# Optimization experiments

Measured on AMD Instinct MI355X. Metric: run time of the kernel, lower is better.

## Reference

```python
import jax, jax.numpy as jnp
import numpy as np

B, STATE_DIM, MLP_DIM, H, W = 128, 64, 512, 40, 40
LN_EPS = 1e-5


def _sobel_kernel(c):
    # Per-channel depthwise filters in torch order: [c0_sx, c0_sy, c0_id, c1_sx, ...]
    sx = jnp.array([[-1., 0., 1.], [-2., 0., 2.], [-1., 0., 1.]], jnp.float32)
    sy = jnp.array([[-1., -2., -1.], [0., 0., 0.], [1., 2., 1.]], jnp.float32)
    ident = jnp.array([[0., 0., 0.], [0., 1., 0.], [0., 0., 0.]], jnp.float32)
    k = jnp.stack([sx, sy, ident])[:, None]      # [3, 1, 3, 3]
    return jnp.tile(k, (c, 1, 1, 1))             # [3c, 1, 3, 3]


def setup_inputs() -> dict:
    key = jax.random.key(0)
    ks = jax.random.split(key, 6)
    state_in = jax.random.normal(ks[0], (B, STATE_DIM, H, W), jnp.float32)
    w1 = jax.random.normal(ks[1], (MLP_DIM, 3 * STATE_DIM), jnp.float32) * 0.05
    ln_weight = jax.random.uniform(ks[2], (MLP_DIM, H, W), jnp.float32, 0.5, 1.5)
    ln_bias = jax.random.normal(ks[3], (MLP_DIM, H, W), jnp.float32) * 0.01
    w2 = jax.random.normal(ks[4], (STATE_DIM, MLP_DIM), jnp.float32) * 0.05
    mask = jax.random.randint(ks[5], (H, W), 0, 2, jnp.int32)  # bernoulli(0.5) update mask
    return {"state_in": state_in, "w1": w1, "ln_weight": ln_weight,
            "ln_bias": ln_bias, "w2": w2, "mask": mask}


def reference(state_in, w1, ln_weight, ln_bias, w2, mask):
    C = state_in.shape[1]
    # Depthwise 3x3 sobel/identity perception: [B, C, H, W] -> [B, 3C, H, W]
    kern = _sobel_kernel(C)
    x = jax.lax.conv_general_dilated(
        state_in, kern, window_strides=(1, 1), padding='SAME',
        dimension_numbers=('NCHW', 'OIHW', 'NCHW'), feature_group_count=C)
    # 1x1 conv (no bias): [B, 3C, H, W] -> [B, MLP, H, W]
    x = jnp.einsum('bchw,oc->bohw', x, w1)
    # LayerNorm over (MLP, H, W) per sample, with elementwise affine
    mu = jnp.mean(x, axis=(1, 2, 3), keepdims=True)
    var = jnp.var(x, axis=(1, 2, 3), keepdims=True)
    x = (x - mu) * jax.lax.rsqrt(var + LN_EPS) * ln_weight + ln_bias
    x = jax.nn.relu(x)
    # 1x1 conv back to state channels (zero-init in original; random here for testing)
    x = jnp.einsum('bchw,oc->bohw', x, w2)
    # Stochastic per-pixel update mask, broadcast over batch and channels
    x = x * mask.astype(jnp.float32)
    # Alive mask: 3x3 max-pool on alive channel, stride 1, SAME padding
    live = jax.lax.reduce_window(state_in[:, 3], -jnp.inf, jax.lax.max,
                                 (1, 3, 3), (1, 1, 1), 'SAME')
    live = (live > 0.1).astype(jnp.float32)[:, None]  # [B, 1, H, W]
    return state_in + x * live
```

## Files before the change

### kernel.cpp

```cpp
#include <hip/hip_runtime.h>


typedef unsigned short u16;
typedef unsigned int   u32;
typedef __attribute__((ext_vector_type(8))) u16    ushort8;
typedef __attribute__((ext_vector_type(4))) u16    u16x4;
typedef __attribute__((ext_vector_type(8))) __bf16 bf16x8;
typedef __attribute__((ext_vector_type(4))) float  f32x4;
typedef __attribute__((ext_vector_type(4))) u32    u32x4;

#define NB   128
#define NC   64
#define K1   192
#define NO   512
#define NHW  1600
#define LN_N 819200.0f

__device__ __forceinline__ u16 f2bf(float f) {
    union { float f; u32 u; } v; v.f = f;
    u32 u = v.u;
    u32 r = u + 0x7fffu + ((u >> 16) & 1u);
    return (u16)(r >> 16);
}
__device__ __forceinline__ float bf2f(u16 h) {
    union { u32 u; float f; } v; v.u = ((u32)h) << 16; return v.f;
}
__device__ __forceinline__ float bfhi(u32 c) {
    union { u32 u; float f; } v; v.u = c & 0xffff0000u; return v.f;
}
__device__ __forceinline__ float bflo(u32 c) {
    union { u32 u; float f; } v; v.u = c << 16; return v.f;
}
__device__ __forceinline__ f32x4 mfma16(bf16x8 a, bf16x8 b, f32x4 c) {
    return __builtin_amdgcn_mfma_f32_16x16x32_bf16(a, b, c, 0, 0, 0);
}
__device__ __forceinline__ bf16x8 ldfrag(const u16* p) {
    return *(const bf16x8*)p;
}

__device__ __forceinline__ void load_halo(const float* __restrict__ base, int h,
                                          int wq, float reg[3][12]) {
#pragma unroll
    for (int jj = 0; jj < 3; ++jj) {
        int hh = h + jj - 1;
        bool vh = (unsigned)hh < 40u;
        const float* rowp = base + hh * 40;
#pragma unroll
        for (int i = 0; i < 12; ++i) {
            int col = wq * 10 - 1 + i;
            reg[jj][i] = (vh && (unsigned)col < 40u) ? rowp[col] : 0.0f;
        }
    }
}
__device__ __forceinline__ void sobel_px(const float reg[3][12], int t,
                                         float& sx, float& sy, float& idn) {
    sx = (reg[0][t + 2] - reg[0][t]) + 2.0f * (reg[1][t + 2] - reg[1][t])
       + (reg[2][t + 2] - reg[2][t]);
    sy = (reg[2][t] + 2.0f * reg[2][t + 1] + reg[2][t + 2])
       - (reg[0][t] + 2.0f * reg[0][t + 1] + reg[0][t + 2]);
    idn = reg[1][t + 1];
}

__global__ __launch_bounds__(256) void k0_convert(const float* __restrict__ w1,
                                                  const float* __restrict__ w2,
                                                  u16* __restrict__ w1p,
                                                  u16* __restrict__ w1T,
                                                  u16* __restrict__ w2p,
                                                  float* __restrict__ stats) {
    int g = blockIdx.x * 256 + threadIdx.x;
    if (g < NO * K1) {
        u16 v = f2bf(w1[g]);
        int o = g / K1, k = g - o * K1;
        int f = o >> 4, ks = k >> 5;
        int lane = (((k >> 3) & 3) << 4) | (o & 15);
        w1p[(size_t)(((f * 6 + ks) * 64 + lane) * 8 + (k & 7))] = v;
        w1T[(size_t)k * NO + o] = v;
    } else if (g < NO * K1 + NC * NO) {
        int i = g - NO * K1;
        int s = i / NO, o = i - s * NO;
        u16 v = f2bf(w2[i]);
        int wid = s >> 4, oc = o >> 6, ks2 = (o >> 5) & 1;
        int lane = (((o >> 3) & 3) << 4) | (s & 15);
        w2p[(size_t)((((wid * 8 + oc) * 2 + ks2) * 64 + lane) * 8 + (o & 7))] = v;
    } else if (g < NO * K1 + NC * NO + 256) {
        stats[g - NO * K1 - NC * NO] = 0.0f;
    }
}

__global__ __launch_bounds__(256) void k0_lncomb(const float* __restrict__ lnw,
                                                 const float* __restrict__ lnb,
                                                 u32* __restrict__ lnp) {
    int g = blockIdx.x * 256 + threadIdx.x;
    int r = g & 3;
    int lane = (g >> 2) & 63;
    int rest = g >> 8;
    int mi = rest % 5;  rest /= 5;
    int wid = rest & 3; rest >>= 2;
    int oc = rest & 7;
    int bx = rest >> 3;
    int p = bx * 80 + mi * 16 + (lane & 15);
    int o = oc * 64 + wid * 16 + ((lane >> 4) << 2) + r;
    size_t gi = (size_t)o * NHW + p;
    lnp[g] = ((u32)f2bf(lnb[gi]) << 16) | f2bf(lnw[gi]);
}

__global__ __launch_bounds__(256) void k0_gram(const u16* __restrict__ w1T,
                                               float* __restrict__ G,
                                               float* __restrict__ colw1) {
    const int blk = blockIdx.x;
    const int tid = threadIdx.x;
    const int lane = tid & 63, wid = tid >> 6;
    const int q = lane >> 4, l15 = lane & 15;
    if (blk < 36) {
        int bj = blk / 6, bk = blk - bj * 6;
        int j0 = bj * 32 + (wid & 1) * 16, k0 = bk * 32 + (wid >> 1) * 16;
        f32x4 acc = {0.f, 0.f, 0.f, 0.f};
#pragma unroll
        for (int ks = 0; ks < 16; ++ks) {
            bf16x8 a  = ldfrag(&w1T[(size_t)(j0 + l15) * NO + ks * 32 + q * 8]);
            bf16x8 bb = ldfrag(&w1T[(size_t)(k0 + l15) * NO + ks * 32 + q * 8]);
            acc = mfma16(a, bb, acc);
        }
#pragma unroll
        for (int r = 0; r < 4; ++r)
            G[(size_t)(j0 + q * 4 + r) * K1 + k0 + l15] = acc[r];
    } else if (tid < K1) {
        float s = 0.f;
        for (int i = 0; i < NO / 8; ++i) {
            ushort8 v = *(const ushort8*)&w1T[(size_t)tid * NO + i * 8];
#pragma unroll
            for (int j = 0; j < 8; ++j) s += bf2f(v[j]);
        }
        colw1[tid] = s;
    }
}

__global__ __launch_bounds__(256) void k2_stats(const float* __restrict__ state,
                                                const float* __restrict__ G,
                                                const float* __restrict__ colw1,
                                                float* __restrict__ stats) {
    const int b = blockIdx.x >> 2, quarter = blockIdx.x & 3;
    const int tid = threadIdx.x;
    const int lane = tid & 63, wid = tid >> 6;
    const int q = lane >> 4, l15 = lane & 15;
    const int j0 = (wid & 1) * 96, j1 = (wid >> 1) * 96, jo = wid * 48;

    __shared__ __align__(16) u16 Pt[208 * 104];
    __shared__ float red[8];

    for (int i = tid; i < 208 * 104 / 2; i += 256) ((u32*)Pt)[i] = 0u;
    __syncthreads();
    if (tid < 80) Pt[192 * 104 + tid] = 0x3F80u;

    f32x4 acc[6][6], accO[3];
#pragma unroll
    for (int i = 0; i < 6; ++i)
#pragma unroll
        for (int j = 0; j < 6; ++j) { f32x4 z = {0.f,0.f,0.f,0.f}; acc[i][j] = z; }
#pragma unroll
    for (int j = 0; j < 3; ++j) { f32x4 z = {0.f,0.f,0.f,0.f}; accO[j] = z; }

    const int c = tid >> 2, wq = tid & 3;
    const float* base = state + ((size_t)b * NC + c) * NHW;

    for (int tile = 0; tile < 5; ++tile) {
        const int h0 = (quarter * 5 + tile) * 2;
        __syncthreads();
        for (int rr = 0; rr < 2; ++rr) {
            float reg[3][12];
            load_halo(base, h0 + rr, wq, reg);
#pragma unroll
            for (int t = 0; t < 10; ++t) {
                float sx, sy, idn; sobel_px(reg, t, sx, sy, idn);
                int px = rr * 40 + wq * 10 + t;
                Pt[(3 * c + 0) * 104 + px] = f2bf(sx);
                Pt[(3 * c + 1) * 104 + px] = f2bf(sy);
                Pt[(3 * c + 2) * 104 + px] = f2bf(idn);
            }
        }
        __syncthreads();
#pragma unroll
        for (int ks = 0; ks < 3; ++ks) {
            bf16x8 av[6], bv[6], ao, bo[3];
#pragma unroll
            for (int fi = 0; fi < 6; ++fi)
                av[fi] = ldfrag(&Pt[(j0 + fi * 16 + l15) * 104 + ks * 32 + q * 8]);
#pragma unroll
            for (int fj = 0; fj < 6; ++fj)
                bv[fj] = ldfrag(&Pt[(j1 + fj * 16 + l15) * 104 + ks * 32 + q * 8]);
            ao = ldfrag(&Pt[(192 + l15) * 104 + ks * 32 + q * 8]);
#pragma unroll
            for (int fj = 0; fj < 3; ++fj)
                bo[fj] = ldfrag(&Pt[(jo + fj * 16 + l15) * 104 + ks * 32 + q * 8]);
#pragma unroll
            for (int fi = 0; fi < 6; ++fi)
#pragma unroll
                for (int fj = 0; fj < 6; ++fj)
                    acc[fi][fj] = mfma16(av[fi], bv[fj], acc[fi][fj]);
#pragma unroll
            for (int fj = 0; fj < 3; ++fj)
                accO[fj] = mfma16(ao, bo[fj], accO[fj]);
        }
    }

    float ssq = 0.f;
#pragma unroll
    for (int fi = 0; fi < 6; ++fi)
#pragma unroll
        for (int fj = 0; fj < 6; ++fj) {
            f32x4 gv = *(const f32x4*)&G[(size_t)(j1 + fj * 16 + l15) * K1
                                         + j0 + fi * 16 + q * 4];
#pragma unroll
            for (int r = 0; r < 4; ++r) ssq += acc[fi][fj][r] * gv[r];
        }
    float sm = 0.f;
    if (q == 0) {
#pragma unroll
        for (int fj = 0; fj < 3; ++fj)
            sm += accO[fj][0] * colw1[jo + fj * 16 + l15];
    }
#pragma unroll
    for (int off = 32; off > 0; off >>= 1) {
        ssq += __shfl_down(ssq, off);
        sm  += __shfl_down(sm, off);
    }
    if (lane == 0) { red[wid] = ssq; red[4 + wid] = sm; }
    __syncthreads();
    if (tid == 0) {
        atomicAdd(&stats[b * 2],     red[4] + red[5] + red[6] + red[7]);
        atomicAdd(&stats[b * 2 + 1], red[0] + red[1] + red[2] + red[3]);
    }
}

__global__ void k3_finalize(const float* __restrict__ stats, float2* __restrict__ musig) {
    int t = threadIdx.x;
    if (t < NB) {
        float s = stats[2 * t], qq = stats[2 * t + 1];
        float inv = 1.0f / LN_N;
        float mu = s * inv;
        float var = qq * inv - mu * mu;
        float2 r; r.x = mu; r.y = rsqrtf(var + 1e-5f);
        musig[t] = r;
    }
}

__global__ __launch_bounds__(256, 4) void k4_fused(const float* __restrict__ state,
                                                   const u16* __restrict__ w1p,
                                                   const u16* __restrict__ w2p,
                                                   const u32* __restrict__ lnp,
                                                   const int* __restrict__ mask,
                                                   const float2* __restrict__ musig,
                                                   float* __restrict__ out) {
    const int bx = blockIdx.x;
    const int b  = blockIdx.y;
    const int p0 = bx * 80, h0 = bx * 2;
    const int tid = threadIdx.x;
    const int lane = tid & 63, wid = tid >> 6;
    const int q = lane >> 4, l15 = lane & 15;

    __shared__ __align__(16) u16 Pt[80 * 192];
    __shared__ __align__(16) u16 Ys[80 * 64];

    const float2 ms = musig[b];
    const float mu = ms.x, rs = ms.y;
    const float murs = mu * rs;

    {
        const int c = tid >> 2, wq = tid & 3;
        const float* base = state + ((size_t)b * NC + c) * NHW;
        for (int rr = 0; rr < 2; ++rr) {
            float reg[3][12];
            load_halo(base, h0 + rr, wq, reg);
#pragma unroll
            for (int t = 0; t < 10; ++t) {
                float sx, sy, idn; sobel_px(reg, t, sx, sy, idn);
                int px = rr * 40 + wq * 10 + t;
                int k = 3 * c;
#pragma unroll
                for (int i = 0; i < 3; ++i) {
                    int kk = k + i, u = kk >> 3;
                    int elem = px * 192 + (((u & 0x18) | ((u ^ px) & 7)) << 3) + (kk & 7);
                    Pt[elem] = f2bf(i == 0 ? sx : (i == 1 ? sy : idn));
                }
            }
        }
    }
    float g5[5];
    {
        const float* st3 = state + ((size_t)b * NC + 3) * NHW;
#pragma unroll
        for (int mi = 0; mi < 5; ++mi) {
            int p = p0 + mi * 16 + l15;
            int h = p / 40, w = p - h * 40;
            float mx = -1e30f;
#pragma unroll
            for (int dh = -1; dh <= 1; ++dh) {
                int hh = h + dh;
                if ((unsigned)hh < 40u)
#pragma unroll
                    for (int dw = -1; dw <= 1; ++dw) {
                        int wc = w + dw;
                        if ((unsigned)wc < 40u) mx = fmaxf(mx, st3[hh * 40 + wc]);
                    }
            }
            g5[mi] = (mx > 0.1f && mask[p] != 0) ? 1.0f : 0.0f;
        }
    }
    __syncthreads();

    f32x4 acc2[5];
#pragma unroll
    for (int i = 0; i < 5; ++i) { f32x4 z = {0.f,0.f,0.f,0.f}; acc2[i] = z; }

    for (int oc = 0; oc < 8; ++oc) {
        u32x4 lv[5];
        {
            const u32* lb = lnp + ((((size_t)bx * 8 + oc) * 4 + wid) * 5) * 256 + lane * 4;
#pragma unroll
            for (int mi = 0; mi < 5; ++mi)
                lv[mi] = *(const u32x4*)(lb + mi * 256);
        }
        const u16* w2base = w2p + ((size_t)(wid * 8 + oc) * 2) * 512 + lane * 8;
        bf16x8 aw0 = ldfrag(w2base);
        bf16x8 aw1 = ldfrag(w2base + 512);

        f32x4 acc1[5];
#pragma unroll
        for (int i = 0; i < 5; ++i) { f32x4 z = {0.f,0.f,0.f,0.f}; acc1[i] = z; }
        const u16* w1base = w1p + ((size_t)(oc * 4 + wid) * 6) * 512 + lane * 8;
#pragma unroll
        for (int ks = 0; ks < 6; ++ks) {
            bf16x8 a = ldfrag(w1base + ks * 512);
#pragma unroll
            for (int mi = 0; mi < 5; ++mi) {
                int r = mi * 16 + l15, u = ks * 4 + q;
                bf16x8 bp = ldfrag(&Pt[r * 192 + (((u & 0x18) | ((u ^ r) & 7)) << 3)]);
                acc1[mi] = mfma16(a, bp, acc1[mi]);
            }
        }
#pragma unroll
        for (int mi = 0; mi < 5; ++mi) {
            int p = mi * 16 + l15;
            u16x4 yv;
#pragma unroll
            for (int r = 0; r < 4; ++r) {
                u32 cc = lv[mi][r];
                float t = fmaf(acc1[mi][r], rs, -murs);
                float y = fmaf(t, bflo(cc), bfhi(cc));
                yv[r] = f2bf(fmaxf(y, 0.0f));
            }
            int u = wid * 2 + (q >> 1);
            int up = u ^ (p & 7);
            *(u16x4*)&Ys[p * 64 + up * 8 + (q & 1) * 4] = yv;
        }
        __syncthreads();
#pragma unroll
        for (int ks2 = 0; ks2 < 2; ++ks2) {
            bf16x8 aw = ks2 ? aw1 : aw0;
#pragma unroll
            for (int mi = 0; mi < 5; ++mi) {
                int p = mi * 16 + l15;
                int u = ks2 * 4 + q;
                int up = u ^ (p & 7);
                bf16x8 by = ldfrag(&Ys[p * 64 + up * 8]);
                acc2[mi] = mfma16(aw, by, acc2[mi]);
            }
        }
        __syncthreads();
    }

#pragma unroll
    for (int mi = 0; mi < 5; ++mi) {
        int p = p0 + mi * 16 + l15;
        float g = g5[mi];
#pragma unroll
        for (int r = 0; r < 4; ++r) {
            int s = wid * 16 + q * 4 + r;
            size_t idx = ((size_t)b * NC + s) * NHW + p;
            out[idx] = state[idx] + g * acc2[mi][r];
        }
    }
}

extern "C" void kernel_launch(void* const* d_in, const int* in_sizes, int n_in,
                              void* d_out, int out_size, void* d_ws, size_t ws_size,
                              hipStream_t stream) {
    const float* state = (const float*)d_in[0];
    const float* w1    = (const float*)d_in[1];
    const float* lnw   = (const float*)d_in[2];
    const float* lnb   = (const float*)d_in[3];
    const float* w2    = (const float*)d_in[4];
    const int*   mask  = (const int*)d_in[5];
    float* out = (float*)d_out;

    char* ws = (char*)d_ws;
    u16*    w1p   = (u16*)(ws + 0ull);
    u16*    w2p   = (u16*)(ws + 196608ull);
    u32*    lnp   = (u32*)(ws + 262144ull);
    u16*    w1T   = (u16*)(ws + 3538944ull);
    float*  G     = (float*)(ws + 3735552ull);
    float*  colw1 = (float*)(ws + 3883008ull);
    float*  stats = (float*)(ws + 3883776ull);
    float2* musig = (float2*)(ws + 3884800ull);

    k0_convert <<<513, 256, 0, stream>>>(w1, w2, w1p, w1T, w2p, stats);
    k0_lncomb  <<<3200, 256, 0, stream>>>(lnw, lnb, lnp);
    k0_gram    <<<37, 256, 0, stream>>>(w1T, G, colw1);
    k2_stats   <<<512, 256, 0, stream>>>(state, G, colw1, stats);
    k3_finalize<<<1, 128, 0, stream>>>(stats, musig);
    k4_fused   <<<dim3(20, 128), 256, 0, stream>>>(state, w1p, w2p, lnp,
                                                   mask, musig, out);
}
```

Measured before the change: 300.8 us.

## Split second GEMM K across waves with per-wave Y tiles and LDS reduction

Each wave now keeps its own 16-channel slice of the hidden activations in a private LDS tile and computes partial products for all 64 output channels. This removes the two block-wide barriers per output-chunk iteration, and the partial sums are reduced through LDS at the end. The w2 layout and a zero-fill kernel are changed to match. The alive-mask computation moves to the epilogue. The cost is four times as many accumulator registers (80 floats), which risks occupancy loss under the 4-block launch bound, plus an extra cross-wave reduction.

```diff
diff --git a/kernel.cpp b/kernel.cpp
--- a/kernel.cpp
+++ b/kernel.cpp
@@ -61,11 +61,16 @@
     idn = reg[1][t + 1];
 }
 
+__global__ __launch_bounds__(256) void k0_zero(u32* __restrict__ w2q32) {
+    int i = blockIdx.x * 256 + threadIdx.x;
+    if (i < 32768) w2q32[i] = 0u;
+}
+
 __global__ __launch_bounds__(256) void k0_convert(const float* __restrict__ w1,
                                                   const float* __restrict__ w2,
                                                   u16* __restrict__ w1p,
                                                   u16* __restrict__ w1T,
-                                                  u16* __restrict__ w2p,
+                                                  u16* __restrict__ w2q,
                                                   float* __restrict__ stats) {
     int g = blockIdx.x * 256 + threadIdx.x;
     if (g < NO * K1) {
@@ -77,11 +82,13 @@
         w1T[(size_t)k * NO + o] = v;
     } else if (g < NO * K1 + NC * NO) {
         int i = g - NO * K1;
-        int s = i / NO, o = i - s * NO;
+        int s = i >> 9, o = i & 511;
         u16 v = f2bf(w2[i]);
-        int wid = s >> 4, oc = o >> 6, ks2 = (o >> 5) & 1;
-        int lane = (((o >> 3) & 3) << 4) | (s & 15);
-        w2p[(size_t)((((wid * 8 + oc) * 2 + ks2) * 64 + lane) * 8 + (o & 7))] = v;
+        int oc = o >> 6, wid = (o >> 4) & 3, k = o & 15;
+        int qq = k >> 3, j = o & 7;
+        int lane = qq * 16 + (s & 15);
+        int sf = s >> 4;
+        w2q[((((size_t)(oc * 4 + sf) * 4 + wid) * 64 + lane) << 3) + j] = v;
     } else if (g < NO * K1 + NC * NO + 256) {
         stats[g - NO * K1 - NC * NO] = 0.0f;
     }
@@ -246,7 +253,7 @@
 
 __global__ __launch_bounds__(256, 4) void k4_fused(const float* __restrict__ state,
                                                    const u16* __restrict__ w1p,
-                                                   const u16* __restrict__ w2p,
+                                                   const u16* __restrict__ w2q,
                                                    const u32* __restrict__ lnp,
                                                    const int* __restrict__ mask,
                                                    const float2* __restrict__ musig,
@@ -258,8 +265,10 @@
     const int lane = tid & 63, wid = tid >> 6;
     const int q = lane >> 4, l15 = lane & 15;
 
-    __shared__ __align__(16) u16 Pt[80 * 192];
-    __shared__ __align__(16) u16 Ys[80 * 64];
+    __shared__ __align__(16) char smem[40960];
+    u16* Pt  = (u16*)smem;
+    u16* Ysw = (u16*)(smem + 30720) + wid * 1280;
+    float* Rd = (float*)smem;
 
     const float2 ms = musig[b];
     const float mu = ms.x, rs = ms.y;
@@ -285,99 +294,180 @@
             }
         }
     }
-    float g5[5];
-    {
-        const float* st3 = state + ((size_t)b * NC + 3) * NHW;
-#pragma unroll
-        for (int mi = 0; mi < 5; ++mi) {
-            int p = p0 + mi * 16 + l15;
-            int h = p / 40, w = p - h * 40;
-            float mx = -1e30f;
-#pragma unroll
-            for (int dh = -1; dh <= 1; ++dh) {
-                int hh = h + dh;
-                if ((unsigned)hh < 40u)
-#pragma unroll
-                    for (int dw = -1; dw <= 1; ++dw) {
-                        int wc = w + dw;
-                        if ((unsigned)wc < 40u) mx = fmaxf(mx, st3[hh * 40 + wc]);
-                    }
-            }
-            g5[mi] = (mx > 0.1f && mask[p] != 0) ? 1.0f : 0.0f;
-        }
-    }
-    __syncthreads();
-
-    f32x4 acc2[5];
-#pragma unroll
-    for (int i = 0; i < 5; ++i) { f32x4 z = {0.f,0.f,0.f,0.f}; acc2[i] = z; }
+    __syncthreads();
+
+    f32x4 acc2[4][5];
+#pragma unroll
+    for (int sf = 0; sf < 4; ++sf)
+#pragma unroll
+        for (int i = 0; i < 5; ++i) { f32x4 z = {0.f,0.f,0.f,0.f}; acc2[sf][i] = z; }
+
+    const int swz = (((l15 >> 2) ^ l15) & 1);
 
     for (int oc = 0; oc < 8; ++oc) {
-        u32x4 lv[5];
+        const u16* w1base = w1p + ((size_t)(oc * 4 + wid) * 6) * 512 + lane * 8;
+        const u32* lbase = lnp + ((((size_t)bx * 8 + oc) * 4 + wid) * 5) * 256 + lane * 4;
+
         {
-            const u32* lb = lnp + ((((size_t)bx * 8 + oc) * 4 + wid) * 5) * 256 + lane * 4;
-#pragma unroll
-            for (int mi = 0; mi < 5; ++mi)
-                lv[mi] = *(const u32x4*)(lb + mi * 256);
-        }
-        const u16* w2base = w2p + ((size_t)(wid * 8 + oc) * 2) * 512 + lane * 8;
-        bf16x8 aw0 = ldfrag(w2base);
-        bf16x8 aw1 = ldfrag(w2base + 512);
-
-        f32x4 acc1[5];
-#pragma unroll
-        for (int i = 0; i < 5; ++i) { f32x4 z = {0.f,0.f,0.f,0.f}; acc1[i] = z; }
-        const u16* w1base = w1p + ((size_t)(oc * 4 + wid) * 6) * 512 + lane * 8;
-#pragma unroll
-        for (int ks = 0; ks < 6; ++ks) {
-            bf16x8 a = ldfrag(w1base + ks * 512);
-#pragma unroll
-            for (int mi = 0; mi < 5; ++mi) {
-                int r = mi * 16 + l15, u = ks * 4 + q;
-                bf16x8 bp = ldfrag(&Pt[r * 192 + (((u & 0x18) | ((u ^ r) & 7)) << 3)]);
-                acc1[mi] = mfma16(a, bp, acc1[mi]);
-            }
-        }
-#pragma unroll
-        for (int mi = 0; mi < 5; ++mi) {
-            int p = mi * 16 + l15;
-            u16x4 yv;
-#pragma unroll
-            for (int r = 0; r < 4; ++r) {
-                u32 cc = lv[mi][r];
-                float t = fmaf(acc1[mi][r], rs, -murs);
-                float y = fmaf(t, bflo(cc), bfhi(cc));
-                yv[r] = f2bf(fmaxf(y, 0.0f));
-            }
-            int u = wid * 2 + (q >> 1);
-            int up = u ^ (p & 7);
-            *(u16x4*)&Ys[p * 64 + up * 8 + (q & 1) * 4] = yv;
-        }
-        __syncthreads();
-#pragma unroll
-        for (int ks2 = 0; ks2 < 2; ++ks2) {
-            bf16x8 aw = ks2 ? aw1 : aw0;
+            f32x4 acc1[3];
+#pragma unroll
+            for (int i = 0; i < 3; ++i) { f32x4 z = {0.f,0.f,0.f,0.f}; acc1[i] = z; }
+#pragma unroll
+            for (int ks = 0; ks < 6; ++ks) {
+                bf16x8 a = ldfrag(w1base + (ks << 9));
+#pragma unroll
+                for (int mi = 0; mi < 3; ++mi) {
+                    int r = mi * 16 + l15, u = ks * 4 + q;
+                    bf16x8 bp = ldfrag(&Pt[r * 192 + (((u & 0x18) | ((u ^ r) & 7)) << 3)]);
+                    acc1[mi] = mfma16(a, bp, acc1[mi]);
+                }
+            }
+#pragma unroll
+            for (int mi = 0; mi < 3; ++mi) {
+                u32x4 lv = *(const u32x4*)(lbase + mi * 256);
+                u16x4 yv;
+#pragma unroll
+                for (int r = 0; r < 4; ++r) {
+                    u32 cc = lv[r];
+                    float t = fmaf(acc1[mi][r], rs, -murs);
+                    float y = fmaf(t, bflo(cc), bfhi(cc));
+                    yv[r] = f2bf(fmaxf(y, 0.0f));
+                }
+                int p = mi * 16 + l15;
+                *(u16x4*)&Ysw[p * 16 + (((q >> 1) ^ swz) << 3) + ((q & 1) << 2)] = yv;
+            }
+        }
+        {
+            f32x4 acc1[2];
+#pragma unroll
+            for (int i = 0; i < 2; ++i) { f32x4 z = {0.f,0.f,0.f,0.f}; acc1[i] = z; }
+#pragma unroll
+            for (int ks = 0; ks < 6; ++ks) {
+                bf16x8 a = ldfrag(w1base + (ks << 9));
+#pragma unroll
+                for (int mi = 0; mi < 2; ++mi) {
+                    int r = (mi + 3) * 16 + l15, u = ks * 4 + q;
+                    bf16x8 bp = ldfrag(&Pt[r * 192 + (((u & 0x18) | ((u ^ r) & 7)) << 3)]);
+                    acc1[mi] = mfma16(a, bp, acc1[mi]);
+                }
+            }
+#pragma unroll
+            for (int mi = 0; mi < 2; ++mi) {
+                u32x4 lv = *(const u32x4*)(lbase + (mi + 3) * 256);
+                u16x4 yv;
+#pragma unroll
+                for (int r = 0; r < 4; ++r) {
+                    u32 cc = lv[r];
+                    float t = fmaf(acc1[mi][r], rs, -murs);
+                    float y = fmaf(t, bflo(cc), bfhi(cc));
+                    yv[r] = f2bf(fmaxf(y, 0.0f));
+                }
+                int p = (mi + 3) * 16 + l15;
+                *(u16x4*)&Ysw[p * 16 + (((q >> 1) ^ swz) << 3) + ((q & 1) << 2)] = yv;
+            }
+        }
+        {
+            bf16x8 aw0 = ldfrag(w2q + (((size_t)(oc * 4 + 0) * 4 + wid) << 9) + lane * 8);
+            bf16x8 aw1 = ldfrag(w2q + (((size_t)(oc * 4 + 1) * 4 + wid) << 9) + lane * 8);
+            bf16x8 aw2 = ldfrag(w2q + (((size_t)(oc * 4 + 2) * 4 + wid) << 9) + lane * 8);
+            bf16x8 aw3 = ldfrag(w2q + (((size_t)(oc * 4 + 3) * 4 + wid) << 9) + lane * 8);
 #pragma unroll
             for (int mi = 0; mi < 5; ++mi) {
                 int p = mi * 16 + l15;
-                int u = ks2 * 4 + q;
-                int up = u ^ (p & 7);
-                bf16x8 by = ldfrag(&Ys[p * 64 + up * 8]);
-                acc2[mi] = mfma16(aw, by, acc2[mi]);
-            }
-        }
-        __syncthreads();
-    }
-
+                bf16x8 by = ldfrag(&Ysw[p * 16 + ((((q & 1) ^ swz)) << 3)]);
+                acc2[0][mi] = mfma16(aw0, by, acc2[0][mi]);
+                acc2[1][mi] = mfma16(aw1, by, acc2[1][mi]);
+                acc2[2][mi] = mfma16(aw2, by, acc2[2][mi]);
+                acc2[3][mi] = mfma16(aw3, by, acc2[3][mi]);
+            }
+        }
+    }
+
+    __syncthreads();
+#pragma unroll
+    for (int sf = 0; sf < 2; ++sf) {
+        if (wid != sf) {
+#pragma unroll
+            for (int mi = 0; mi < 5; ++mi)
+                *(f32x4*)(Rd + (size_t)(sf * 4 + wid) * 1280 + mi * 256 + lane * 4)
+                    = acc2[sf][mi];
+        }
+    }
+    __syncthreads();
+#pragma unroll
+    for (int sf = 0; sf < 2; ++sf) {
+        if (wid == sf) {
+#pragma unroll
+            for (int w = 0; w < 4; ++w) {
+                if (w == sf) continue;
+#pragma unroll
+                for (int mi = 0; mi < 5; ++mi) {
+                    f32x4 v = *(const f32x4*)(Rd + (size_t)(sf * 4 + w) * 1280
+                                              + mi * 256 + lane * 4);
+#pragma unroll
+                    for (int r = 0; r < 4; ++r) acc2[sf][mi][r] += v[r];
+                }
+            }
+        }
+    }
+    __syncthreads();
+#pragma unroll
+    for (int sf = 2; sf < 4; ++sf) {
+        if (wid != sf) {
+#pragma unroll
+            for (int mi = 0; mi < 5; ++mi)
+                *(f32x4*)(Rd + (size_t)((sf - 2) * 4 + wid) * 1280 + mi * 256 + lane * 4)
+                    = acc2[sf][mi];
+        }
+    }
+    __syncthreads();
+#pragma unroll
+    for (int sf = 2; sf < 4; ++sf) {
+        if (wid == sf) {
+#pragma unroll
+            for (int w = 0; w < 4; ++w) {
+                if (w == sf) continue;
+#pragma unroll
+                for (int mi = 0; mi < 5; ++mi) {
+                    f32x4 v = *(const f32x4*)(Rd + (size_t)((sf - 2) * 4 + w) * 1280
+                                              + mi * 256 + lane * 4);
+#pragma unroll
+                    for (int r = 0; r < 4; ++r) acc2[sf][mi][r] += v[r];
+                }
+            }
+        }
+    }
+
+    f32x4 accO[5];
+#pragma unroll
+    for (int sf = 0; sf < 4; ++sf)
+        if (wid == sf) {
+#pragma unroll
+            for (int mi = 0; mi < 5; ++mi) accO[mi] = acc2[sf][mi];
+        }
+
+    const float* st3 = state + ((size_t)b * NC + 3) * NHW;
 #pragma unroll
     for (int mi = 0; mi < 5; ++mi) {
         int p = p0 + mi * 16 + l15;
-        float g = g5[mi];
+        int h = p / 40, w = p - h * 40;
+        float mx = -1e30f;
+#pragma unroll
+        for (int dh = -1; dh <= 1; ++dh) {
+            int hh = h + dh;
+            if ((unsigned)hh < 40u)
+#pragma unroll
+                for (int dw = -1; dw <= 1; ++dw) {
+                    int wc = w + dw;
+                    if ((unsigned)wc < 40u) mx = fmaxf(mx, st3[hh * 40 + wc]);
+                }
+        }
+        float g = (mx > 0.1f && mask[p] != 0) ? 1.0f : 0.0f;
 #pragma unroll
         for (int r = 0; r < 4; ++r) {
             int s = wid * 16 + q * 4 + r;
             size_t idx = ((size_t)b * NC + s) * NHW + p;
-            out[idx] = state[idx] + g * acc2[mi][r];
+            out[idx] = state[idx] + g * accO[mi][r];
         }
     }
 }
@@ -395,19 +485,20 @@
 
     char* ws = (char*)d_ws;
     u16*    w1p   = (u16*)(ws + 0ull);
-    u16*    w2p   = (u16*)(ws + 196608ull);
-    u32*    lnp   = (u32*)(ws + 262144ull);
-    u16*    w1T   = (u16*)(ws + 3538944ull);
-    float*  G     = (float*)(ws + 3735552ull);
-    float*  colw1 = (float*)(ws + 3883008ull);
-    float*  stats = (float*)(ws + 3883776ull);
-    float2* musig = (float2*)(ws + 3884800ull);
-
-    k0_convert <<<513, 256, 0, stream>>>(w1, w2, w1p, w1T, w2p, stats);
+    u16*    w2q   = (u16*)(ws + 196608ull);
+    u32*    lnp   = (u32*)(ws + 327680ull);
+    u16*    w1T   = (u16*)(ws + 3604480ull);
+    float*  G     = (float*)(ws + 3801088ull);
+    float*  colw1 = (float*)(ws + 3948544ull);
+    float*  stats = (float*)(ws + 3949312ull);
+    float2* musig = (float2*)(ws + 3950336ull);
+
+    k0_zero    <<<128, 256, 0, stream>>>((u32*)w2q);
+    k0_convert <<<513, 256, 0, stream>>>(w1, w2, w1p, w1T, w2q, stats);
     k0_lncomb  <<<3200, 256, 0, stream>>>(lnw, lnb, lnp);
     k0_gram    <<<37, 256, 0, stream>>>(w1T, G, colw1);
     k2_stats   <<<512, 256, 0, stream>>>(state, G, colw1, stats);
     k3_finalize<<<1, 128, 0, stream>>>(stats, musig);
-    k4_fused   <<<dim3(20, 128), 256, 0, stream>>>(state, w1p, w2p, lnp,
+    k4_fused   <<<dim3(20, 128), 256, 0, stream>>>(state, w1p, w2q, lnp,
                                                    mask, musig, out);
 }
```

Result: slower. 341.4 us (+13.5%).
